# Performance work log

Hardware: AMD Instinct MI355X
Metric: run time of the kernel (lower is better)

## Reference

```python
import jax, jax.numpy as jnp
import numpy as np
from jax import lax

B, L, H = 2, 4096, 2048
NH = 16
DK = H // NH  # num_slot = 128 (q/k dim)
C = 64        # chunk size
EPS = 1e-5
N_LAYER = 24


def setup_inputs() -> dict:
    key = jax.random.key(0)
    ks = jax.random.split(key, 7)
    std = 0.02
    return {
        "hidden_states": jax.random.normal(ks[0], (B, L, H), jnp.float32),
        "Wq": jax.random.normal(ks[1], (DK, H), jnp.float32) * std,
        "Wk": jax.random.normal(ks[2], (DK, H), jnp.float32) * std,
        "Wog": jax.random.normal(ks[3], (H, H), jnp.float32) * std,
        "Wig": jax.random.normal(ks[4], (H, H), jnp.float32) * std,
        "Wo": jax.random.normal(ks[5], (H, H), jnp.float32) * (std / np.sqrt(2 * N_LAYER)),
        "g_norm_w": jnp.ones((H,), jnp.float32),
    }


def _gla_chunk(q, k, v, gf):
    # q,k,gf: [b,L,dk]; v: [b,L,dv]. Recurrence: S_t = diag(exp(gf_t)) S_{t-1} + k_t v_t^T; o_t = q_t S_t
    b, Ls, dk = q.shape
    dv = v.shape[-1]
    n = Ls // C
    # [n, b, C, d] so scan iterates over chunks
    qc = q.reshape(b, n, C, dk).transpose(1, 0, 2, 3)
    kc = k.reshape(b, n, C, dk).transpose(1, 0, 2, 3)
    vc = v.reshape(b, n, C, dv).transpose(1, 0, 2, 3)
    gc = gf.reshape(b, n, C, dk).transpose(1, 0, 2, 3)
    Bc = jnp.cumsum(gc, axis=2)  # inclusive within-chunk log-decay

    tril = jnp.tril(jnp.ones((C, C), bool))

    def step(S, inp):
        qh, kh, vh, Bh = inp  # [b,C,dk],[b,C,dk],[b,C,dv],[b,C,dk]
        Blast = Bh[:, -1, :]  # [b,dk]
        # exp(B_i - B_j) <= 1 for j <= i (gf < 0): numerically safe pairwise form
        D = Bh[:, :, None, :] - Bh[:, None, :, :]  # [b,C,C,dk]
        A = jnp.einsum('bid,bjd,bijd->bij', qh, kh, jnp.exp(D))
        A = jnp.where(tril, A, 0.0)
        o_intra = jnp.einsum('bij,bjv->biv', A, vh)
        o_inter = jnp.einsum('bid,bdv->biv', qh * jnp.exp(Bh), S)
        kd = kh * jnp.exp(Blast[:, None, :] - Bh)  # <= 1 scaling, safe
        S_new = S * jnp.exp(Blast)[..., None] + jnp.einsum('bjd,bjv->bdv', kd, vh)
        return S_new, o_intra + o_inter

    S0 = jnp.zeros((b, dk, dv), q.dtype)
    _, o = lax.scan(step, S0, (qc, kc, vc, Bc))  # o: [n,b,C,dv]
    return o.transpose(1, 0, 2, 3).reshape(b, Ls, dv)


def reference(hidden_states, Wq, Wk, Wog, Wig, Wo, g_norm_w):
    x = hidden_states
    q = jax.nn.softmax(x @ Wq.T, axis=-1)        # [b,L,dk]
    k = jax.nn.sigmoid(x @ Wk.T)                 # [b,L,dk]
    v = x                                        # value_dim == hidden_size
    gf = jax.nn.log_sigmoid(-k)                  # per-key-dim log decay, in (-1.32, -0.69)
    o = _gla_chunk(q, k, v, gf)                  # [b,L,H]
    # output gate: og_proj(o) + ig_proj(x), fused RMSNorm + swish gate
    go = o @ Wog.T + x @ Wig.T
    on = o * lax.rsqrt(jnp.mean(o * o, axis=-1, keepdims=True) + EPS) * g_norm_w
    o = on * (go * jax.nn.sigmoid(go))
    return o @ Wo.T
```

## Files before the change

kernel.cpp:

```cpp
#include <hip/hip_runtime.h>
#include <hip/hip_bf16.h>

typedef __hip_bfloat16 bf16;
typedef __bf16 bf16x8 __attribute__((ext_vector_type(8)));
typedef float f32x4 __attribute__((ext_vector_type(4)));

__device__ __forceinline__ void async16(void* lds_base, const void* g) {
  __builtin_amdgcn_global_load_lds(
      (const __attribute__((address_space(1))) void*)g,
      (__attribute__((address_space(3))) void*)lds_base, 16, 0, 0);
}

__global__ void cvt_bf16_kernel(const float* __restrict__ s, bf16* __restrict__ d, int n4) {
  const int i = blockIdx.x * 256 + threadIdx.x;
  if (i >= n4) return;
  const float4 v = ((const float4*)s)[i];
  bf16 h0 = __float2bfloat16(v.x), h1 = __float2bfloat16(v.y);
  bf16 h2 = __float2bfloat16(v.z), h3 = __float2bfloat16(v.w);
  ushort4 o;
  o.x = *(unsigned short*)&h0; o.y = *(unsigned short*)&h1;
  o.z = *(unsigned short*)&h2; o.w = *(unsigned short*)&h3;
  *(ushort4*)((unsigned short*)d + (size_t)i * 4) = o;
}

__global__ void cvt_bf16_strided(const float* __restrict__ s, bf16* __restrict__ d, int n4) {
  const int i = blockIdx.x * 256 + threadIdx.x;
  if (i >= n4) return;
  const int row = i >> 9;
  const int col4 = i & 511;
  const float4 v = ((const float4*)s)[i];
  bf16 h0 = __float2bfloat16(v.x), h1 = __float2bfloat16(v.y);
  bf16 h2 = __float2bfloat16(v.z), h3 = __float2bfloat16(v.w);
  ushort4 o;
  o.x = *(unsigned short*)&h0; o.y = *(unsigned short*)&h1;
  o.z = *(unsigned short*)&h2; o.w = *(unsigned short*)&h3;
  *(ushort4*)((unsigned short*)d + (size_t)row * 4096 + col4 * 4) = o;
}

__global__ __launch_bounds__(256) void convert_x_kernel(
    const float* __restrict__ x, bf16* __restrict__ comb, bf16* __restrict__ xbT) {
  __shared__ float tile[64][65];
  const int b = blockIdx.z;
  const int l0 = blockIdx.x * 64, d0 = blockIdx.y * 64;
  const int t = threadIdx.x;
  const int c4 = (t & 15) * 4, r = t >> 4;
  const size_t base = ((size_t)b * 4096 + l0) * 2048 + d0;
#pragma unroll
  for (int i = 0; i < 4; ++i) {
    const int row = i * 16 + r;
    const float4 v = *(const float4*)(x + base + (size_t)row * 2048 + c4);
    tile[row][c4 + 0] = v.x; tile[row][c4 + 1] = v.y;
    tile[row][c4 + 2] = v.z; tile[row][c4 + 3] = v.w;
    bf16 h0 = __float2bfloat16(v.x), h1 = __float2bfloat16(v.y);
    bf16 h2 = __float2bfloat16(v.z), h3 = __float2bfloat16(v.w);
    ushort4 o;
    o.x = *(unsigned short*)&h0; o.y = *(unsigned short*)&h1;
    o.z = *(unsigned short*)&h2; o.w = *(unsigned short*)&h3;
    *(ushort4*)(comb + ((size_t)(b * 4096 + l0 + row)) * 4096 + 2048 + d0 + c4) = o;
  }
  __syncthreads();
#pragma unroll
  for (int i = 0; i < 4; ++i) {
    const int d = i * 16 + r;
    bf16 h0 = __float2bfloat16(tile[c4 + 0][d]);
    bf16 h1 = __float2bfloat16(tile[c4 + 1][d]);
    bf16 h2 = __float2bfloat16(tile[c4 + 2][d]);
    bf16 h3 = __float2bfloat16(tile[c4 + 3][d]);
    ushort4 o;
    o.x = *(unsigned short*)&h0; o.y = *(unsigned short*)&h1;
    o.z = *(unsigned short*)&h2; o.w = *(unsigned short*)&h3;
    *(ushort4*)(xbT + ((size_t)(b * 2048 + d0 + d)) * 4096 + l0 + c4) = o;
  }
}

__global__ __launch_bounds__(256, 2) void gemm_logits(
    const bf16* __restrict__ A, const bf16* __restrict__ B,
    float* __restrict__ outf, int lda, int N, int K) {
  __shared__ bf16 lA[128 * 32];
  __shared__ bf16 lB[128 * 32];
  const int tid = threadIdx.x;
  const int lane = tid & 63, wave = tid >> 6;
  const int l15 = lane & 15, l4 = lane >> 4;
  const int bm = blockIdx.x * 128, bn = blockIdx.y * 128;
  const int wm = (wave & 1) * 64, wn = (wave >> 1) * 64;
  const int srow = tid >> 2;
  const int skc = (tid & 3) * 8;

  const f32x4 fz = {0.f, 0.f, 0.f, 0.f};
  f32x4 acc[4][4];
#pragma unroll
  for (int i = 0; i < 4; ++i)
#pragma unroll
    for (int j = 0; j < 4; ++j) acc[i][j] = fz;

  bf16* lAu  = lA + wave * 512;
  bf16* lAu2 = lA + 2048 + wave * 512;
  bf16* lBu  = lB + wave * 512;
  bf16* lBu2 = lB + 2048 + wave * 512;

  const bf16* gA0 = A + (size_t)(bm + srow) * lda + skc;
  const bf16* gA1 = A + (size_t)(bm + srow + 64) * lda + skc;
  const bf16* gB0 = B + (size_t)(bn + srow) * K + skc;
  const bf16* gB1 = B + (size_t)(bn + srow + 64) * K + skc;
  for (int k0 = 0; k0 < K; k0 += 32) {
    __syncthreads();
    async16(lAu, gA0 + k0);
    async16(lAu2, gA1 + k0);
    async16(lBu, gB0 + k0);
    async16(lBu2, gB1 + k0);
    __syncthreads();
    bf16x8 af[4], bfv[4];
#pragma unroll
    for (int mt = 0; mt < 4; ++mt)
      af[mt] = *(const bf16x8*)(lA + (wm + mt * 16 + l15) * 32 + l4 * 8);
#pragma unroll
    for (int nt = 0; nt < 4; ++nt)
      bfv[nt] = *(const bf16x8*)(lB + (wn + nt * 16 + l15) * 32 + l4 * 8);
#pragma unroll
    for (int mt = 0; mt < 4; ++mt)
#pragma unroll
      for (int nt = 0; nt < 4; ++nt)
        acc[mt][nt] = __builtin_amdgcn_mfma_f32_16x16x32_bf16(af[mt], bfv[nt], acc[mt][nt], 0, 0, 0);
  }

#pragma unroll
  for (int mt = 0; mt < 4; ++mt)
#pragma unroll
    for (int r = 0; r < 4; ++r) {
      const int gr = bm + wm + mt * 16 + l4 * 4 + r;
#pragma unroll
      for (int nt = 0; nt < 4; ++nt) {
        const int gc = bn + wn + nt * 16 + l15;
        outf[(size_t)gr * N + gc] = acc[mt][nt][r];
      }
    }
}

#define QMFMA(AF, BF, MH, NH)                                               \
  do {                                                                      \
    __builtin_amdgcn_s_setprio(1);                                          \
    _Pragma("unroll") for (int ks_ = 0; ks_ < 2; ++ks_) {                   \
      _Pragma("unroll") for (int mt_ = 0; mt_ < 4; ++mt_) {                 \
        _Pragma("unroll") for (int nt_ = 0; nt_ < 2; ++nt_)                 \
            acc[(MH) * 4 + mt_][(NH) * 2 + nt_] =                           \
                __builtin_amdgcn_mfma_f32_16x16x32_bf16(                    \
                    AF[mt_][ks_], BF[nt_][ks_],                             \
                    acc[(MH) * 4 + mt_][(NH) * 2 + nt_], 0, 0, 0);          \
      }                                                                     \
    }                                                                       \
    __builtin_amdgcn_s_setprio(0);                                          \
  } while (0)

template <int MODE>
__global__ __launch_bounds__(512, 2) void gemm256(
    const bf16* __restrict__ A, const bf16* __restrict__ B,
    float* __restrict__ outf, bf16* __restrict__ outb,
    const bf16* __restrict__ o_in, const float* __restrict__ rmssum,
    const float* __restrict__ gnw, int N, int K, int ostr) {
  __shared__ bf16 lA[2][16384];
  __shared__ bf16 lB[2][16384];
  const int tid = threadIdx.x;
  const int lane = tid & 63;
  const int wave = tid >> 6;
  const int wmi = wave >> 2;
  const int wni = wave & 3;
  const int l15 = lane & 15, l4 = lane >> 4;
  const int axor = l15 & 7;

  const int nwg = gridDim.x;
  const int cpx = nwg >> 3;
  int wg = blockIdx.x;
  wg = (wg & 7) * cpx + (wg >> 3);
  const int NBN = N >> 8;
  const int bm = (wg / NBN) * 256;
  const int bn = (wg % NBN) * 256;

  const int srow = tid >> 3;
  const int scol = ((tid & 7) ^ (srow & 7)) * 8;
  const size_t goff = (size_t)srow * K + scol;
  const int NT = K >> 6;

  const bf16* Ab = A + (size_t)bm * K + goff;
  const bf16* Bb = B + (size_t)bn * K + goff;

  auto stageA = [&](int kt, int h, int buf) {
    const int t = (kt < NT) ? kt : (NT - 1);
    const bf16* g = Ab + (size_t)h * 128 * K + t * 64;
    bf16* d = &lA[buf][h * 8192] + tid * 8;
    async16(d, g);
    async16(d + 4096, g + (size_t)64 * K);
  };
  auto stageB = [&](int kt, int h, int buf) {
    const int t = (kt < NT) ? kt : (NT - 1);
    const bf16* g = Bb + (size_t)h * 128 * K + t * 64;
    bf16* d = &lB[buf][h * 8192] + tid * 8;
    async16(d, g);
    async16(d + 4096, g + (size_t)64 * K);
  };

  auto readA = [&](bf16x8 (&af)[4][2], int buf, int mh) {
    const bf16* base = &lA[buf][wmi * 8192];
#pragma unroll
    for (int mt = 0; mt < 4; ++mt)
#pragma unroll
      for (int ks = 0; ks < 2; ++ks)
        af[mt][ks] = *(const bf16x8*)(base + (mh * 64 + mt * 16 + l15) * 64 +
                                      (((ks * 4 + l4) ^ axor) << 3));
  };
  auto readB = [&](bf16x8 (&bb)[2][2], int buf, int nh) {
    const bf16* base = &lB[buf][(wni >> 1) * 8192];
#pragma unroll
    for (int nt = 0; nt < 2; ++nt)
#pragma unroll
      for (int ks = 0; ks < 2; ++ks)
        bb[nt][ks] = *(const bf16x8*)(base +
                                      ((wni & 1) * 64 + nh * 32 + nt * 16 + l15) * 64 +
                                      (((ks * 4 + l4) ^ axor) << 3));
  };

  const f32x4 fz = {0.f, 0.f, 0.f, 0.f};
  f32x4 acc[8][4];
#pragma unroll
  for (int i = 0; i < 8; ++i)
#pragma unroll
    for (int j = 0; j < 4; ++j) acc[i][j] = fz;

  stageB(0, 0, 0); stageB(0, 1, 0);
  stageA(0, 0, 0); stageA(0, 1, 0);
  stageB(1, 0, 1); stageB(1, 1, 1);
  asm volatile("s_waitcnt vmcnt(4)" ::: "memory");
  __builtin_amdgcn_s_barrier();
  __builtin_amdgcn_sched_barrier(0);

  bf16x8 aF[4][2], b0F[2][2], b1F[2][2];

  auto ktile = [&](int kt, int cur, int nxt) {
    readA(aF, cur, 0);
    readB(b0F, cur, 0);
    stageA(kt + 1, 0, nxt);
    asm volatile("s_waitcnt lgkmcnt(8)" ::: "memory");
    __builtin_amdgcn_s_barrier();
    asm volatile("s_waitcnt lgkmcnt(0)" ::: "memory");
    QMFMA(aF, b0F, 0, 0);
    __builtin_amdgcn_s_barrier();
    readB(b1F, cur, 1);
    stageA(kt + 1, 1, nxt);
    __builtin_amdgcn_s_barrier();
    asm volatile("s_waitcnt lgkmcnt(0)" ::: "memory");
    QMFMA(aF, b1F, 0, 1);
    __builtin_amdgcn_s_barrier();
    readA(aF, cur, 1);
    stageB(kt + 2, 0, cur);
    __builtin_amdgcn_s_barrier();
    asm volatile("s_waitcnt lgkmcnt(0)" ::: "memory");
    QMFMA(aF, b0F, 1, 0);
    __builtin_amdgcn_s_barrier();
    stageB(kt + 2, 1, cur);
    asm volatile("s_waitcnt vmcnt(4)" ::: "memory");
    __builtin_amdgcn_s_barrier();
    __builtin_amdgcn_sched_barrier(0);
    QMFMA(aF, b1F, 1, 1);
    __builtin_amdgcn_s_barrier();
  };

  for (int kt = 0; kt < NT; kt += 2) {
    ktile(kt, 0, 1);
    ktile(kt + 1, 1, 0);
  }

#pragma unroll
  for (int i = 0; i < 8; ++i) {
#pragma unroll
    for (int r = 0; r < 4; ++r) {
      const int gr = bm + wmi * 128 + i * 16 + l4 * 4 + r;
      float rinv = 0.f;
      if (MODE == 1) rinv = rsqrtf(rmssum[gr] * (1.f / 2048.f) + 1e-5f);
#pragma unroll
      for (int j = 0; j < 4; ++j) {
        const int gc = bn + wni * 64 + j * 16 + l15;
        const float v = acc[i][j][r];
        if (MODE == 1) {
          const float o = (float)o_in[(size_t)gr * ostr + gc];
          const float on = o * rinv * gnw[gc];
          const float sw = v / (1.f + __expf(-v));
          outb[(size_t)gr * N + gc] = __float2bfloat16(on * sw);
        } else {
          outf[(size_t)gr * N + gc] = v;
        }
      }
    }
  }
}

__global__ __launch_bounds__(64) void qk_post_kernel(
    const float* __restrict__ logits, bf16* __restrict__ qb,
    bf16* __restrict__ kb, float* __restrict__ gfl, float* __restrict__ rmssum) {
  const int row = blockIdx.x;
  const int t = threadIdx.x;
  if (t == 0) rmssum[row] = 0.f;
  const float* lr = logits + (size_t)row * 256;
  float a0 = lr[t], a1 = lr[t + 64];
  float m = fmaxf(a0, a1);
#pragma unroll
  for (int s = 32; s; s >>= 1) m = fmaxf(m, __shfl_xor(m, s));
  float e0 = __expf(a0 - m), e1 = __expf(a1 - m);
  float sum = e0 + e1;
#pragma unroll
  for (int s = 32; s; s >>= 1) sum += __shfl_xor(sum, s);
  const float inv = 1.f / sum;
  qb[(size_t)row * 128 + t]      = __float2bfloat16(e0 * inv);
  qb[(size_t)row * 128 + t + 64] = __float2bfloat16(e1 * inv);
  float b0 = lr[128 + t], b1 = lr[128 + t + 64];
  float k0 = 1.f / (1.f + __expf(-b0));
  float k1 = 1.f / (1.f + __expf(-b1));
  kb[(size_t)row * 128 + t]      = __float2bfloat16(k0);
  kb[(size_t)row * 128 + t + 64] = __float2bfloat16(k1);
  gfl[(size_t)row * 128 + t]      = -log1pf(__expf(k0));
  gfl[(size_t)row * 128 + t + 64] = -log1pf(__expf(k1));
}

__global__ __launch_bounds__(256, 2) void gla_kernel(
    const bf16* __restrict__ qb, const bf16* __restrict__ kb,
    const float* __restrict__ gfl, const bf16* __restrict__ xbT,
    bf16* __restrict__ ob, float* __restrict__ rmssum) {
  __shared__ bf16 sF1[64][136];
  __shared__ bf16 sF2[128][136];
  __shared__ float sM[128];
  __shared__ float rowsq[64];
  const int tid = threadIdx.x;
  const int lane = tid & 63, wave = tid >> 6;
  const int l15 = lane & 15, l4 = lane >> 4;
  const int chunk = blockIdx.x, b = blockIdx.y, z = blockIdx.z;
  const int row0 = b * 4096 + chunk * 64;

  if (tid < 64) rowsq[tid] = 0.f;

  if (tid < 128) {
    float s = 0.f;
    for (int i = 0; i <= 32; ++i) s += gfl[(size_t)(row0 + i) * 128 + tid];
    sM[tid] = s;
  }
  __syncthreads();

  if (tid < 128) {
    const int d = tid;
    const float M = sM[d];
    float bi = 0.f;
    for (int i = 0; i < 64; ++i) {
      bi += gfl[(size_t)(row0 + i) * 128 + d];
      const float q = (float)qb[(size_t)(row0 + i) * 128 + d];
      const float k = (float)kb[(size_t)(row0 + i) * 128 + d];
      sF1[i][d]      = __float2bfloat16(q * __expf(bi - M));
      sF2[64 + i][d] = __float2bfloat16(k * __expf(M - bi));
    }
  } else {
    const int d = tid - 128;
    if (chunk == 0) {
      for (int j = 0; j < 64; ++j) sF2[j][d] = __float2bfloat16(0.f);
    } else {
      const float M = sM[d];
      float bw = 0.f;
      for (int j = 63; j >= 0; --j) {
        const float k = (float)kb[(size_t)(row0 - 64 + j) * 128 + d];
        sF2[j][d] = __float2bfloat16(k * __expf(M - bw));
        bw -= gfl[(size_t)(row0 - 64 + j) * 128 + d];
      }
    }
  }
  __syncthreads();

  const f32x4 fz = {0.f, 0.f, 0.f, 0.f};
  {
    f32x4 sacc[4][2];
#pragma unroll
    for (int mt = 0; mt < 4; ++mt) { sacc[mt][0] = fz; sacc[mt][1] = fz; }
    bf16x8 f1[4][4];
#pragma unroll
    for (int kt = 0; kt < 4; ++kt)
#pragma unroll
      for (int mt = 0; mt < 4; ++mt)
        f1[kt][mt] = *(const bf16x8*)(&sF1[mt * 16 + l15][kt * 32 + l4 * 8]);
#pragma unroll
    for (int nt = 0; nt < 2; ++nt)
#pragma unroll
      for (int kt = 0; kt < 4; ++kt) {
        const bf16x8 f2 = *(const bf16x8*)(&sF2[wave * 32 + nt * 16 + l15][kt * 32 + l4 * 8]);
#pragma unroll
        for (int mt = 0; mt < 4; ++mt)
          sacc[mt][nt] = __builtin_amdgcn_mfma_f32_16x16x32_bf16(f1[kt][mt], f2, sacc[mt][nt], 0, 0, 0);
      }
    __syncthreads();
#pragma unroll
    for (int mt = 0; mt < 4; ++mt)
#pragma unroll
      for (int nt = 0; nt < 2; ++nt)
#pragma unroll
        for (int r = 0; r < 4; ++r) {
          const int i = mt * 16 + l4 * 4 + r;
          const int jw = wave * 32 + nt * 16 + l15;
          const bool ok = (jw < 64) || (jw - 64 <= i);
          sF1[i][jw] = __float2bfloat16(ok ? sacc[mt][nt][r] : 0.f);
        }
    __syncthreads();
  }

  bf16x8 av[4][4];
#pragma unroll
  for (int kt = 0; kt < 4; ++kt)
#pragma unroll
    for (int mt = 0; mt < 4; ++mt)
      av[kt][mt] = *(const bf16x8*)(&sF1[mt * 16 + l15][kt * 32 + l4 * 8]);

  float rs[4][4];
#pragma unroll
  for (int a = 0; a < 4; ++a)
#pragma unroll
    for (int r2 = 0; r2 < 4; ++r2) rs[a][r2] = 0.f;

  const int lwb = chunk * 64 - 64;
  for (int dt = z * 4; dt < z * 4 + 4; ++dt) {
    const int c0 = dt * 256 + wave * 64;
    f32x4 oacc[4][4];
#pragma unroll
    for (int mt = 0; mt < 4; ++mt)
#pragma unroll
      for (int nt = 0; nt < 4; ++nt) oacc[mt][nt] = fz;
#pragma unroll
    for (int kt = 0; kt < 4; ++kt)
#pragma unroll
      for (int nt = 0; nt < 4; ++nt) {
        const int dv = c0 + nt * 16 + l15;
        int lw = lwb + kt * 32 + l4 * 8;
        if (lw < 0) lw = 0;
        const bf16x8 vv = *(const bf16x8*)(xbT + ((size_t)b * 2048 + dv) * 4096 + lw);
#pragma unroll
        for (int mt = 0; mt < 4; ++mt)
          oacc[mt][nt] = __builtin_amdgcn_mfma_f32_16x16x32_bf16(av[kt][mt], vv, oacc[mt][nt], 0, 0, 0);
      }
#pragma unroll
    for (int mt = 0; mt < 4; ++mt)
#pragma unroll
      for (int r = 0; r < 4; ++r) {
        const int i = mt * 16 + l4 * 4 + r;
#pragma unroll
        for (int nt = 0; nt < 4; ++nt) {
          const float v = oacc[mt][nt][r];
          ob[(size_t)(row0 + i) * 4096 + (c0 + nt * 16 + l15)] = __float2bfloat16(v);
          rs[mt][r] += v * v;
        }
      }
  }

#pragma unroll
  for (int mt = 0; mt < 4; ++mt)
#pragma unroll
    for (int r = 0; r < 4; ++r) {
      float v = rs[mt][r];
      v += __shfl_xor(v, 1); v += __shfl_xor(v, 2);
      v += __shfl_xor(v, 4); v += __shfl_xor(v, 8);
      if (l15 == 0) atomicAdd(&rowsq[mt * 16 + l4 * 4 + r], v);
    }
  __syncthreads();
  if (tid < 64)
    atomicAdd(&rmssum[row0 + tid], rowsq[tid]);
}

extern "C" void kernel_launch(void* const* d_in, const int* in_sizes, int n_in,
                              void* d_out, int out_size, void* d_ws, size_t ws_size,
                              hipStream_t stream) {
  const float* x   = (const float*)d_in[0];
  const float* Wq  = (const float*)d_in[1];
  const float* Wk  = (const float*)d_in[2];
  const float* Wog = (const float*)d_in[3];
  const float* Wig = (const float*)d_in[4];
  const float* Wo  = (const float*)d_in[5];
  const float* gnw = (const float*)d_in[6];
  float* out = (float*)d_out;

  char* w = (char*)d_ws;
  auto alloc = [&](size_t bytes) {
    char* p = w;
    w += (bytes + 255) & ~(size_t)255;
    return p;
  };
  bf16*  wqkb   = (bf16*)alloc((size_t)256 * 2048 * 2);
  bf16*  wcomb  = (bf16*)alloc((size_t)2048 * 4096 * 2);
  bf16*  wob    = (bf16*)alloc((size_t)2048 * 2048 * 2);
  bf16*  acomb  = (bf16*)alloc((size_t)8192 * 4096 * 2);
  bf16*  xbT    = (bf16*)alloc((size_t)8192 * 2048 * 2);
  float* logits = (float*)alloc((size_t)8192 * 256 * 4);
  bf16*  qbuf   = (bf16*)alloc((size_t)8192 * 128 * 2);
  bf16*  kbuf   = (bf16*)alloc((size_t)8192 * 128 * 2);
  float* gfbuf  = (float*)alloc((size_t)8192 * 128 * 4);
  float* rmsbuf = (float*)alloc((size_t)8192 * 4);
  bf16*  gatedb = xbT;

  cvt_bf16_kernel<<<dim3((65536 + 255) / 256), 256, 0, stream>>>(Wq, wqkb, 65536);
  cvt_bf16_kernel<<<dim3((65536 + 255) / 256), 256, 0, stream>>>(Wk, wqkb + 262144, 65536);
  cvt_bf16_strided<<<dim3((1048576 + 255) / 256), 256, 0, stream>>>(Wog, wcomb, 1048576);
  cvt_bf16_strided<<<dim3((1048576 + 255) / 256), 256, 0, stream>>>(Wig, wcomb + 2048, 1048576);
  cvt_bf16_kernel<<<dim3((1048576 + 255) / 256), 256, 0, stream>>>(Wo, wob, 1048576);

  convert_x_kernel<<<dim3(64, 32, 2), 256, 0, stream>>>(x, acomb, xbT);

  gemm_logits<<<dim3(64, 2), 256, 0, stream>>>(
      acomb + 2048, wqkb, logits, 4096, 256, 2048);

  qk_post_kernel<<<dim3(8192), 64, 0, stream>>>(logits, qbuf, kbuf, gfbuf, rmsbuf);

  gla_kernel<<<dim3(64, 2, 2), 256, 0, stream>>>(qbuf, kbuf, gfbuf, xbT, acomb, rmsbuf);

  gemm256<1><<<dim3(256), 512, 0, stream>>>(
      acomb, wcomb, nullptr, gatedb, acomb, rmsbuf, gnw, 2048, 4096, 4096);

  gemm256<2><<<dim3(256), 512, 0, stream>>>(
      gatedb, wob, out, nullptr, nullptr, nullptr, nullptr, 2048, 2048, 2048);

  (void)in_sizes; (void)n_in; (void)out_size; (void)ws_size;
}
```

Baseline: 473.3 us.

## Restructure GEMM main loop into deeper prefetch pipeline with double-buffered register fragments

Rewrites the k-tile loop of the GEMM kernel so that LDS-to-register reads for the next MFMA quarter are issued before the current quarter's MFMAs, using separate register sets for the two A halves and two B halves. Global-to-LDS staging is pushed two k-tiles ahead, with adjusted vmcnt/lgkmcnt thresholds so waits are partial rather than full drains. This is meant to hide LDS read and global load latency behind MFMA work. In exchange it raises register pressure, and it depends on the hand-tuned wait counts being correct. A final full drain is added after the loop.

```diff
diff --git a/kernel.cpp b/kernel.cpp
--- a/kernel.cpp
+++ b/kernel.cpp
@@ -225,41 +225,52 @@
 #pragma unroll
     for (int j = 0; j < 4; ++j) acc[i][j] = fz;
 
-  stageB(0, 0, 0); stageB(0, 1, 0);
-  stageA(0, 0, 0); stageA(0, 1, 0);
-  stageB(1, 0, 1); stageB(1, 1, 1);
-  asm volatile("s_waitcnt vmcnt(4)" ::: "memory");
+  bf16x8 aH0[4][2], aH1[4][2], b0[2][2], b1[2][2];
+
+  stageA(0, 0, 0); stageA(0, 1, 0); stageB(0, 0, 0); stageB(0, 1, 0);
+  stageA(1, 0, 1); stageB(1, 0, 1); stageB(1, 1, 1); stageA(1, 1, 1);
+  asm volatile("s_waitcnt vmcnt(8)" ::: "memory");
   __builtin_amdgcn_s_barrier();
+  readA(aH0, 0, 0);
+  readB(b0, 0, 0);
   __builtin_amdgcn_sched_barrier(0);
 
-  bf16x8 aF[4][2], b0F[2][2], b1F[2][2];
-
   auto ktile = [&](int kt, int cur, int nxt) {
-    readA(aF, cur, 0);
-    readB(b0F, cur, 0);
-    stageA(kt + 1, 0, nxt);
+    readB(b1, cur, 1);
+    __builtin_amdgcn_sched_barrier(0);
+    __builtin_amdgcn_s_barrier();
+    asm volatile("s_waitcnt lgkmcnt(4)" ::: "memory");
+    __builtin_amdgcn_sched_barrier(0);
+    QMFMA(aH0, b0, 0, 0);
+    asm volatile("s_waitcnt vmcnt(8)" ::: "memory");
+    __builtin_amdgcn_s_barrier();
+    readA(aH1, cur, 1);
+    stageA(kt + 2, 0, cur);
+    __builtin_amdgcn_sched_barrier(0);
+    __builtin_amdgcn_s_barrier();
     asm volatile("s_waitcnt lgkmcnt(8)" ::: "memory");
-    __builtin_amdgcn_s_barrier();
-    asm volatile("s_waitcnt lgkmcnt(0)" ::: "memory");
-    QMFMA(aF, b0F, 0, 0);
-    __builtin_amdgcn_s_barrier();
-    readB(b1F, cur, 1);
-    stageA(kt + 1, 1, nxt);
-    __builtin_amdgcn_s_barrier();
-    asm volatile("s_waitcnt lgkmcnt(0)" ::: "memory");
-    QMFMA(aF, b1F, 0, 1);
-    __builtin_amdgcn_s_barrier();
-    readA(aF, cur, 1);
+    __builtin_amdgcn_sched_barrier(0);
+    QMFMA(aH0, b1, 0, 1);
+    asm volatile("s_waitcnt vmcnt(8)" ::: "memory");
+    __builtin_amdgcn_s_barrier();
+    readA(aH0, nxt, 0);
     stageB(kt + 2, 0, cur);
-    __builtin_amdgcn_s_barrier();
-    asm volatile("s_waitcnt lgkmcnt(0)" ::: "memory");
-    QMFMA(aF, b0F, 1, 0);
-    __builtin_amdgcn_s_barrier();
     stageB(kt + 2, 1, cur);
-    asm volatile("s_waitcnt vmcnt(4)" ::: "memory");
-    __builtin_amdgcn_s_barrier();
-    __builtin_amdgcn_sched_barrier(0);
-    QMFMA(aF, b1F, 1, 1);
+    __builtin_amdgcn_sched_barrier(0);
+    __builtin_amdgcn_s_barrier();
+    asm volatile("s_waitcnt lgkmcnt(8)" ::: "memory");
+    __builtin_amdgcn_sched_barrier(0);
+    QMFMA(aH1, b0, 1, 0);
+    asm volatile("s_waitcnt vmcnt(10)" ::: "memory");
+    __builtin_amdgcn_s_barrier();
+    readB(b0, nxt, 0);
+    stageA(kt + 2, 1, cur);
+    __builtin_amdgcn_sched_barrier(0);
+    __builtin_amdgcn_s_barrier();
+    asm volatile("s_waitcnt lgkmcnt(12)" ::: "memory");
+    __builtin_amdgcn_sched_barrier(0);
+    QMFMA(aH1, b1, 1, 1);
+    asm volatile("s_waitcnt vmcnt(10)" ::: "memory");
     __builtin_amdgcn_s_barrier();
   };
 
@@ -267,6 +278,8 @@
     ktile(kt, 0, 1);
     ktile(kt + 1, 1, 0);
   }
+  asm volatile("s_waitcnt vmcnt(0) lgkmcnt(0)" ::: "memory");
+  __builtin_amdgcn_s_barrier();
 
 #pragma unroll
   for (int i = 0; i < 8; ++i) {
```

New measurement: 444.9 us. 1.06x faster.
